# Optimization experiments

Hardware: AMD Instinct MI355X
Metric: run time of the kernel (lower is better)

## Reference

```python
import jax, jax.numpy as jnp
import numpy as np

S = 8192      # total patch tokens
NSEG = 8      # number of images/segments (equal length)
D = 1280      # embed dim
H = 16        # heads
HD = 80       # head dim
MLP = 3456    # swiglu hidden


def setup_inputs() -> dict:
    key = jax.random.key(0)
    ks = jax.random.split(key, 8)
    def w(k, shape):
        return jax.random.normal(k, shape, jnp.float32) * 0.02
    return {
        "x": jax.random.normal(ks[0], (S, 1, D), jnp.float32),
        "rotary_pos_emb": jax.random.uniform(ks[1], (S, HD // 2), jnp.float32) * 6.2831853,
        "cu_seqlens": jnp.arange(NSEG + 1, dtype=jnp.int32) * (S // NSEG),
        "norm1_w": jnp.ones((D,), jnp.float32), "norm1_b": jnp.zeros((D,), jnp.float32),
        "norm2_w": jnp.ones((D,), jnp.float32), "norm2_b": jnp.zeros((D,), jnp.float32),
        "w_qkv": w(ks[2], (3 * D, D)), "b_qkv": jnp.zeros((3 * D,), jnp.float32),
        "w_proj": w(ks[3], (D, D)), "b_proj": jnp.zeros((D,), jnp.float32),
        "w_gate": w(ks[4], (MLP, D)), "b_gate": jnp.zeros((MLP,), jnp.float32),
        "w_up": w(ks[5], (MLP, D)), "b_up": jnp.zeros((MLP,), jnp.float32),
        "w_down": w(ks[6], (D, MLP)), "b_down": jnp.zeros((D,), jnp.float32),
    }


def _ln(x, w, b, eps=1e-6):
    m = x.mean(-1, keepdims=True)
    v = ((x - m) ** 2).mean(-1, keepdims=True)
    return (x - m) * jax.lax.rsqrt(v + eps) * w + b


def _rope(x, cos, sin):
    # x: [B, S, H, HD]; cos/sin: [S, HD/2]; non-interleaved (chunk-halves) rotation
    c = jnp.concatenate([cos, cos], -1)[None, :, None, :]
    s = jnp.concatenate([sin, sin], -1)[None, :, None, :]
    x1, x2 = jnp.split(x, 2, -1)
    return x * c + jnp.concatenate([-x2, x1], -1) * s


def _forward(cu, x, freqs, norm1_w, norm1_b, norm2_w, norm2_b,
             w_qkv, b_qkv, w_proj, b_proj,
             w_gate, b_gate, w_up, b_up, w_down, b_down):
    S_, B, D_ = x.shape  # B == 1
    L = int(cu[1] - cu[0])          # equal-length segments
    nseg = len(cu) - 1
    h = _ln(x, norm1_w, norm1_b)
    qkv = h @ w_qkv.T + b_qkv                                   # [S, B, 3D]
    q, k, v = jnp.split(qkv, 3, -1)
    q, k, v = (t.reshape(S_, B, H, HD).transpose(1, 0, 2, 3) for t in (q, k, v))  # [B,S,H,d]
    cos, sin = jnp.cos(freqs), jnp.sin(freqs)
    q = _rope(q, cos, sin)
    k = _rope(k, cos, sin)
    # block-diagonal attention over cu_seqlens: fold segments into batch
    qs, ks_, vs = (t.reshape(B * nseg, L, H, HD) for t in (q, k, v))
    scale = 1.0 / np.float32(np.sqrt(HD))
    scores = jnp.einsum('blhd,bmhd->bhlm', qs, ks_) * scale     # [nseg,H,L,L]
    attn = jax.nn.softmax(scores, axis=-1)
    ctx = jnp.einsum('bhlm,bmhd->blhd', attn, vs)               # [nseg,L,H,d]
    ctx = ctx.reshape(B, S_, H * HD).transpose(1, 0, 2)         # [S,B,D]
    x = x + ctx @ w_proj.T + b_proj
    h2 = _ln(x, norm2_w, norm2_b)
    gate = jax.nn.silu(h2 @ w_gate.T + b_gate)
    up = h2 @ w_up.T + b_up
    return x + (gate * up) @ w_down.T + b_down


def reference(x, rotary_pos_emb, cu_seqlens, norm1_w, norm1_b, norm2_w, norm2_b,
              w_qkv, b_qkv, w_proj, b_proj, w_gate, b_gate, w_up, b_up,
              w_down, b_down):
    cu = np.asarray(cu_seqlens)
    return _forward(cu, x, rotary_pos_emb, norm1_w, norm1_b, norm2_w, norm2_b,
                    w_qkv, b_qkv, w_proj, b_proj,
                    w_gate, b_gate, w_up, b_up, w_down, b_down)
```

## Files before the change

kernel.cpp:

```cpp
#include <hip/hip_runtime.h>


#define S_TOK 8192
#define DIM   1280
#define NHEAD 16
#define HDIM  80
#define SEGLEN 1024
#define MLPD  3456

typedef __attribute__((ext_vector_type(8))) short bf16x8;
typedef __attribute__((ext_vector_type(8))) unsigned short u16x8;
typedef __attribute__((ext_vector_type(4))) float f32x4;

__device__ __forceinline__ float bf2f(unsigned short u) {
    unsigned int x = ((unsigned int)u) << 16;
    return __builtin_bit_cast(float, x);
}
__device__ __forceinline__ unsigned short f2bf(float f) {
    unsigned int x = __builtin_bit_cast(unsigned int, f);
    unsigned int r = x + 0x7fffu + ((x >> 16) & 1u);
    return (unsigned short)(r >> 16);
}

__device__ __forceinline__ void gload_lds16(const void* g, void* l) {
    __builtin_amdgcn_global_load_lds(
        (const __attribute__((address_space(1))) void*)g,
        (__attribute__((address_space(3))) void*)l, 16, 0, 0);
}

__device__ __forceinline__ int xcd_swz(int bid, int nwg) {
    const int q = nwg >> 3, r = nwg & 7;
    const int x = bid & 7, j = bid >> 3;
    return (x < r ? x * (q + 1) : r * (q + 1) + (x - r) * q) + j;
}

__global__ __launch_bounds__(256)
void f2b_kernel(const float* __restrict__ in, unsigned short* __restrict__ out, int n4)
{
    const int i = blockIdx.x * 256 + threadIdx.x;
    if (i >= n4) return;
    const float4 v = ((const float4*)in)[i];
    ushort4 o;
    o.x = f2bf(v.x); o.y = f2bf(v.y); o.z = f2bf(v.z); o.w = f2bf(v.w);
    ((ushort4*)out)[i] = o;
}

__global__ __launch_bounds__(256)
void ln_kernel(const float* __restrict__ xin,
               const float* __restrict__ w,
               const float* __restrict__ b,
               unsigned short* __restrict__ out)
{
    const int row = blockIdx.x;
    const int t = threadIdx.x;
    const size_t base = (size_t)row * DIM;
    float v[5];
#pragma unroll
    for (int i = 0; i < 5; ++i) v[i] = xin[base + t + i * 256];
    float s = 0.f, s2 = 0.f;
#pragma unroll
    for (int i = 0; i < 5; ++i) { s += v[i]; s2 += v[i] * v[i]; }
#pragma unroll
    for (int off = 32; off > 0; off >>= 1) {
        s  += __shfl_down(s, off);
        s2 += __shfl_down(s2, off);
    }
    __shared__ float rs[8];
    const int wave = t >> 6, lane = t & 63;
    if (lane == 0) { rs[wave] = s; rs[wave + 4] = s2; }
    __syncthreads();
    s  = rs[0] + rs[1] + rs[2] + rs[3];
    s2 = rs[4] + rs[5] + rs[6] + rs[7];
    const float mean = s * (1.f / DIM);
    const float var  = s2 * (1.f / DIM) - mean * mean;
    const float rstd = rsqrtf(var + 1e-6f);
#pragma unroll
    for (int i = 0; i < 5; ++i) {
        const int c = t + i * 256;
        out[base + c] = f2bf((v[i] - mean) * rstd * w[c] + b[c]);
    }
}

__global__ __launch_bounds__(256)
void rope_kernel(const unsigned short* __restrict__ qkv,
                 const float* __restrict__ rot,
                 unsigned short* __restrict__ qr,
                 unsigned short* __restrict__ kr)
{
    const int idx = blockIdx.x * 256 + threadIdx.x;
    const int s = idx / DIM, rem = idx % DIM;
    const int h = rem / HDIM, d = rem % HDIM;
    const int dd = (d < 40) ? d : d - 40;
    const float th = rot[s * 40 + dd];
    const float c = __cosf(th), sn = __sinf(th);
    const size_t base = (size_t)s * (3 * DIM) + h * HDIM;
    const int partner = (d < 40) ? d + 40 : d - 40;
    const float sgn = (d < 40) ? -1.f : 1.f;
    const float q  = bf2f(qkv[base + d]);
    const float k  = bf2f(qkv[DIM + base + d]);
    const float qp = bf2f(qkv[base + partner]);
    const float kp = bf2f(qkv[DIM + base + partner]);
    const float qo = q * c + sgn * qp * sn;
    const float ko = k * c + sgn * kp * sn;
    qr[idx] = f2bf(qo * 0.11180339887498949f);
    kr[idx] = f2bf(ko);
}

enum { EPI_BF16 = 0, EPI_PROJ = 1, EPI_DOWN = 3 };

template<int EPI>
__global__ __launch_bounds__(512)
void gemm2p(const unsigned short* __restrict__ A,
            const unsigned short* __restrict__ B,
            const float* __restrict__ bias,
            void* __restrict__ C,
            const void* __restrict__ aux,
            int M, int N, int K, int ntn)
{
    __shared__ __align__(16) unsigned short As[2][256 * 32];
    __shared__ __align__(16) unsigned short Bs[2][128 * 32];
    const int t = threadIdx.x;
    const int wave = t >> 6, lane = t & 63;
    const int m = lane & 15, g = lane >> 4;
    const int wr = wave >> 1, wc = wave & 1;
    const int wg = xcd_swz(blockIdx.x, gridDim.x);
    const int n0 = (wg % ntn) * 128;
    const int m0 = (wg / ntn) * 256;

    f32x4 acc[4][4] = {};
    const int nk = K >> 5;

    auto STAGE = [&](int b, int kt) {
        const int k0 = kt << 5;
#pragma unroll
        for (int i = 0; i < 2; ++i) {
            const int ch = i * 512 + t;
            const int row = ch >> 2, cc = ch & 3;
            gload_lds16(A + (size_t)(m0 + row) * K + k0 + cc * 8, &As[b][ch * 8]);
        }
        {
            const int row = t >> 2, cc = t & 3;
            gload_lds16(B + (size_t)(n0 + row) * K + k0 + cc * 8, &Bs[b][t * 8]);
        }
    };

    STAGE(0, 0);
    __syncthreads();
    int cur = 0;
    for (int kt = 0; kt < nk; ++kt) {
        if (kt + 1 < nk) STAGE(cur ^ 1, kt + 1);
        bf16x8 af[4], bfv[4];
#pragma unroll
        for (int mm = 0; mm < 4; ++mm)
            af[mm] = *(const bf16x8*)&As[cur][(wr * 64 + mm * 16 + m) * 32 + g * 8];
#pragma unroll
        for (int nn = 0; nn < 4; ++nn)
            bfv[nn] = *(const bf16x8*)&Bs[cur][(wc * 64 + nn * 16 + m) * 32 + g * 8];
#pragma unroll
        for (int mm = 0; mm < 4; ++mm)
#pragma unroll
            for (int nn = 0; nn < 4; ++nn)
                acc[mm][nn] = __builtin_amdgcn_mfma_f32_16x16x32_bf16(
                    af[mm], bfv[nn], acc[mm][nn], 0, 0, 0);
        __syncthreads();
        cur ^= 1;
    }

#pragma unroll
    for (int mm = 0; mm < 4; ++mm) {
        const int row = m0 + wr * 64 + mm * 16 + g * 4;
#pragma unroll
        for (int nn = 0; nn < 4; ++nn) {
            const int col = n0 + wc * 64 + nn * 16 + m;
            const float bv = bias[col];
#pragma unroll
            for (int i = 0; i < 4; ++i) {
                const int r = row + i;
                const float v = acc[mm][nn][i] + bv;
                const size_t idx = (size_t)r * N + col;
                if (EPI == EPI_BF16) {
                    ((unsigned short*)C)[idx] = f2bf(v);
                } else if (EPI == EPI_PROJ) {
                    const float xr = ((const float*)aux)[idx];
                    ((float*)C)[idx] = v + xr;
                } else {
                    const float xr = ((const float*)aux)[idx];
                    ((float*)C)[idx] = v + xr;
                }
            }
        }
    }
}

__global__ __launch_bounds__(512)
void gemm2p_gu(const unsigned short* __restrict__ A,
               const unsigned short* __restrict__ Bg,
               const unsigned short* __restrict__ Bu,
               const float* __restrict__ bg,
               const float* __restrict__ bu,
               unsigned short* __restrict__ C,
               int M, int N, int K, int ntn)
{
    __shared__ __align__(16) unsigned short As[2][256 * 32];
    __shared__ __align__(16) unsigned short Gs[2][128 * 32];
    __shared__ __align__(16) unsigned short Us[2][128 * 32];
    const int t = threadIdx.x;
    const int wave = t >> 6, lane = t & 63;
    const int m = lane & 15, g = lane >> 4;
    const int wr = wave >> 1, wc = wave & 1;
    const int wg = xcd_swz(blockIdx.x, gridDim.x);
    const int n0 = (wg % ntn) * 128;
    const int m0 = (wg / ntn) * 256;

    f32x4 accg[4][4] = {}, accu[4][4] = {};
    const int nk = K >> 5;

    auto STAGE = [&](int b, int kt) {
        const int k0 = kt << 5;
#pragma unroll
        for (int i = 0; i < 2; ++i) {
            const int ch = i * 512 + t;
            const int row = ch >> 2, cc = ch & 3;
            gload_lds16(A + (size_t)(m0 + row) * K + k0 + cc * 8, &As[b][ch * 8]);
        }
        {
            const int row = t >> 2, cc = t & 3;
            gload_lds16(Bg + (size_t)(n0 + row) * K + k0 + cc * 8, &Gs[b][t * 8]);
            gload_lds16(Bu + (size_t)(n0 + row) * K + k0 + cc * 8, &Us[b][t * 8]);
        }
    };

    STAGE(0, 0);
    __syncthreads();
    int cur = 0;
    for (int kt = 0; kt < nk; ++kt) {
        if (kt + 1 < nk) STAGE(cur ^ 1, kt + 1);
        bf16x8 af[4], gf[4], uf[4];
#pragma unroll
        for (int mm = 0; mm < 4; ++mm)
            af[mm] = *(const bf16x8*)&As[cur][(wr * 64 + mm * 16 + m) * 32 + g * 8];
#pragma unroll
        for (int nn = 0; nn < 4; ++nn) {
            gf[nn] = *(const bf16x8*)&Gs[cur][(wc * 64 + nn * 16 + m) * 32 + g * 8];
            uf[nn] = *(const bf16x8*)&Us[cur][(wc * 64 + nn * 16 + m) * 32 + g * 8];
        }
#pragma unroll
        for (int mm = 0; mm < 4; ++mm)
#pragma unroll
            for (int nn = 0; nn < 4; ++nn) {
                accg[mm][nn] = __builtin_amdgcn_mfma_f32_16x16x32_bf16(
                    af[mm], gf[nn], accg[mm][nn], 0, 0, 0);
                accu[mm][nn] = __builtin_amdgcn_mfma_f32_16x16x32_bf16(
                    af[mm], uf[nn], accu[mm][nn], 0, 0, 0);
            }
        __syncthreads();
        cur ^= 1;
    }

#pragma unroll
    for (int mm = 0; mm < 4; ++mm) {
        const int row = m0 + wr * 64 + mm * 16 + g * 4;
#pragma unroll
        for (int nn = 0; nn < 4; ++nn) {
            const int col = n0 + wc * 64 + nn * 16 + m;
            const float bgv = bg[col], buv = bu[col];
#pragma unroll
            for (int i = 0; i < 4; ++i) {
                const float gv = accg[mm][nn][i] + bgv;
                const float uv = accu[mm][nn][i] + buv;
                const float sg = gv / (1.f + __expf(-gv));
                C[(size_t)(row + i) * N + col] = f2bf(sg * uv);
            }
        }
    }
}

__global__ __launch_bounds__(256)
void attn_mfma_kernel(const unsigned short* __restrict__ qr,
                      const unsigned short* __restrict__ kr,
                      const unsigned short* __restrict__ qkv,
                      unsigned short* __restrict__ ctx)
{
    const int qt = blockIdx.x, hh = blockIdx.y, seg = blockIdx.z;
    const int t = threadIdx.x;
    const int w = t >> 6, lane = t & 63;
    const int m = lane & 15, g = lane >> 4;

    __shared__ __align__(16) unsigned short Ks[64 * 80];
    __shared__ __align__(16) unsigned short Vt[80 * 72];
    __shared__ __align__(16) unsigned short Ps[4][16 * 72];

    const int q0 = seg * SEGLEN + qt * 64 + w * 16;

    bf16x8 qa0, qa1, qa2 = {};
    {
        const unsigned short* qrow = qr + (size_t)(q0 + m) * DIM + hh * HDIM;
        qa0 = *(const bf16x8*)(qrow + 8 * g);
        qa1 = *(const bf16x8*)(qrow + 32 + 8 * g);
        if (g < 2) qa2 = *(const bf16x8*)(qrow + 64 + 8 * g);
    }

    f32x4 o[5] = {};
    float mrow[4], lrow[4];
#pragma unroll
    for (int i = 0; i < 4; ++i) { mrow[i] = -1e30f; lrow[i] = 0.f; }

    for (int kt = 0; kt < SEGLEN / 64; ++kt) {
        const int kbase = seg * SEGLEN + kt * 64;
#pragma unroll
        for (int i = 0; i < 2; ++i) {
            const int ch = t + 256 * i;
            const int row = ch / 10, c = ch % 10;
            gload_lds16(kr + (size_t)(kbase + row) * DIM + hh * HDIM + c * 8,
                        &Ks[ch * 8]);
        }
        if (t < 128) {
            const int ch = 512 + t;
            const int row = ch / 10, c = ch % 10;
            gload_lds16(kr + (size_t)(kbase + row) * DIM + hh * HDIM + c * 8,
                        &Ks[ch * 8]);
        }
#pragma unroll
        for (int i = 0; i < 3; ++i) {
            const int ch = t + 256 * i;
            if (ch < 640) {
                const int k = ch & 63, dc = ch >> 6;
                const u16x8 v = *(const u16x8*)(qkv +
                    (size_t)(kbase + k) * (3 * DIM) + 2 * DIM + hh * HDIM + dc * 8);
#pragma unroll
                for (int e = 0; e < 8; ++e)
                    Vt[(dc * 8 + e) * 72 + k] = v[e];
            }
        }
        __syncthreads();

        f32x4 s[4] = {};
#pragma unroll
        for (int nn = 0; nn < 4; ++nn) {
            const unsigned short* kb = &Ks[(16 * nn + m) * 80];
            const bf16x8 b0 = *(const bf16x8*)(kb + 8 * g);
            const bf16x8 b1 = *(const bf16x8*)(kb + 32 + 8 * g);
            bf16x8 b2 = {};
            if (g < 2) b2 = *(const bf16x8*)(kb + 64 + 8 * g);
            s[nn] = __builtin_amdgcn_mfma_f32_16x16x32_bf16(qa0, b0, s[nn], 0, 0, 0);
            s[nn] = __builtin_amdgcn_mfma_f32_16x16x32_bf16(qa1, b1, s[nn], 0, 0, 0);
            s[nn] = __builtin_amdgcn_mfma_f32_16x16x32_bf16(qa2, b2, s[nn], 0, 0, 0);
        }

#pragma unroll
        for (int i = 0; i < 4; ++i) {
            float mx = fmaxf(fmaxf(s[0][i], s[1][i]), fmaxf(s[2][i], s[3][i]));
            mx = fmaxf(mx, __shfl_xor(mx, 1));
            mx = fmaxf(mx, __shfl_xor(mx, 2));
            mx = fmaxf(mx, __shfl_xor(mx, 4));
            mx = fmaxf(mx, __shfl_xor(mx, 8));
            const float mn = fmaxf(mrow[i], mx);
            const float fs = __expf(mrow[i] - mn);
            float rs = 0.f;
#pragma unroll
            for (int nn = 0; nn < 4; ++nn) {
                const float p = __expf(s[nn][i] - mn);
                s[nn][i] = p;
                rs += p;
            }
            rs += __shfl_xor(rs, 1);
            rs += __shfl_xor(rs, 2);
            rs += __shfl_xor(rs, 4);
            rs += __shfl_xor(rs, 8);
            lrow[i] = lrow[i] * fs + rs;
            mrow[i] = mn;
#pragma unroll
            for (int df = 0; df < 5; ++df) o[df][i] *= fs;
        }

#pragma unroll
        for (int nn = 0; nn < 4; ++nn)
#pragma unroll
            for (int i = 0; i < 4; ++i)
                Ps[w][(4 * g + i) * 72 + 16 * nn + m] = f2bf(s[nn][i]);

        const bf16x8 pa0 = *(const bf16x8*)&Ps[w][m * 72 + 8 * g];
        const bf16x8 pa1 = *(const bf16x8*)&Ps[w][m * 72 + 32 + 8 * g];
#pragma unroll
        for (int df = 0; df < 5; ++df) {
            const unsigned short* vb = &Vt[(16 * df + m) * 72];
            const bf16x8 vb0 = *(const bf16x8*)(vb + 8 * g);
            const bf16x8 vb1 = *(const bf16x8*)(vb + 32 + 8 * g);
            o[df] = __builtin_amdgcn_mfma_f32_16x16x32_bf16(pa0, vb0, o[df], 0, 0, 0);
            o[df] = __builtin_amdgcn_mfma_f32_16x16x32_bf16(pa1, vb1, o[df], 0, 0, 0);
        }
        __syncthreads();
    }

#pragma unroll
    for (int i = 0; i < 4; ++i) {
        const float inv = 1.f / lrow[i];
        unsigned short* crow = ctx + (size_t)(q0 + 4 * g + i) * DIM + hh * HDIM;
#pragma unroll
        for (int df = 0; df < 5; ++df)
            crow[16 * df + m] = f2bf(o[df][i] * inv);
    }
}

extern "C" void kernel_launch(void* const* d_in, const int* in_sizes, int n_in,
                              void* d_out, int out_size, void* d_ws, size_t ws_size,
                              hipStream_t stream)
{
    const float* x      = (const float*)d_in[0];
    const float* rot    = (const float*)d_in[1];
    const float* n1w    = (const float*)d_in[3];
    const float* n1b    = (const float*)d_in[4];
    const float* n2w    = (const float*)d_in[5];
    const float* n2b    = (const float*)d_in[6];
    const float* w_qkv  = (const float*)d_in[7];
    const float* b_qkv  = (const float*)d_in[8];
    const float* w_proj = (const float*)d_in[9];
    const float* b_proj = (const float*)d_in[10];
    const float* w_gate = (const float*)d_in[11];
    const float* b_gate = (const float*)d_in[12];
    const float* w_up   = (const float*)d_in[13];
    const float* b_up   = (const float*)d_in[14];
    const float* w_down = (const float*)d_in[15];
    const float* b_down = (const float*)d_in[16];

    char* ws = (char*)d_ws;
    unsigned short* qkv  = (unsigned short*)(ws + 0);
    unsigned short* h    = (unsigned short*)(ws + 62914560ull);
    unsigned short* qr   = (unsigned short*)(ws + 83886080ull);
    unsigned short* kr   = (unsigned short*)(ws + 104857600ull);
    unsigned short* ctx  = (unsigned short*)(ws + 125829120ull);
    float*          x2   = (float*)(ws + 146800640ull);
    unsigned short* wqb  = (unsigned short*)(ws + 188743680ull);
    unsigned short* wpb  = (unsigned short*)(ws + 198574080ull);
    unsigned short* wgb  = (unsigned short*)(ws + 201850880ull);
    unsigned short* wub  = (unsigned short*)(ws + 210698240ull);
    unsigned short* wdb  = (unsigned short*)(ws + 219545600ull);
    unsigned short* gbuf = qkv;

    {
        const int nq = 3 * DIM * DIM / 4, np = DIM * DIM / 4, nm = MLPD * DIM / 4;
        f2b_kernel<<<(nq + 255) / 256, 256, 0, stream>>>(w_qkv,  wqb, nq);
        f2b_kernel<<<(np + 255) / 256, 256, 0, stream>>>(w_proj, wpb, np);
        f2b_kernel<<<(nm + 255) / 256, 256, 0, stream>>>(w_gate, wgb, nm);
        f2b_kernel<<<(nm + 255) / 256, 256, 0, stream>>>(w_up,   wub, nm);
        f2b_kernel<<<(nm + 255) / 256, 256, 0, stream>>>(w_down, wdb, nm);
    }

    ln_kernel<<<S_TOK, 256, 0, stream>>>(x, n1w, n1b, h);
    gemm2p<EPI_BF16><<<(3 * DIM / 128) * (S_TOK / 256), 512, 0, stream>>>(
        h, wqb, b_qkv, qkv, nullptr, S_TOK, 3 * DIM, DIM, 3 * DIM / 128);
    rope_kernel<<<(S_TOK * DIM) / 256, 256, 0, stream>>>(qkv, rot, qr, kr);
    attn_mfma_kernel<<<dim3(SEGLEN / 64, NHEAD, S_TOK / SEGLEN), 256, 0, stream>>>(
        qr, kr, qkv, ctx);
    gemm2p<EPI_PROJ><<<(DIM / 128) * (S_TOK / 256), 512, 0, stream>>>(
        ctx, wpb, b_proj, x2, x, S_TOK, DIM, DIM, DIM / 128);
    ln_kernel<<<S_TOK, 256, 0, stream>>>(x2, n2w, n2b, h);
    gemm2p_gu<<<(MLPD / 128) * (S_TOK / 256), 512, 0, stream>>>(
        h, wgb, wub, b_gate, b_up, gbuf, S_TOK, MLPD, DIM, MLPD / 128);
    gemm2p<EPI_DOWN><<<(DIM / 128) * (S_TOK / 256), 512, 0, stream>>>(
        gbuf, wdb, b_down, (float*)d_out, x2, S_TOK, DIM, MLPD, DIM / 128);
}
```

Baseline: 682.0 us.

## Rework GEMMs with 4-stage LDS pipeline, XOR swizzle, and larger per-wave tiles

Replaces the double-buffered GEMM kernels with a four-slot ring in dynamic shared memory, keeping three k-tiles of global-to-LDS loads in flight through explicit vmcnt waits. It also XOR-swizzles the LDS layout to cut bank conflicts, regroups the eight waves as 2x4 so each wave computes 128 rows with more MFMAs per fragment load, widens the QKV tile to 256 columns, and raises wave priority around the MFMA block. The larger LDS footprint (up to 128KB) and accumulator count may lower occupancy and raise register pressure.

Measured after the change: 677.6 us. Within noise of the previous version (-0.7%).

```diff
diff --git a/kernel.cpp b/kernel.cpp
--- a/kernel.cpp
+++ b/kernel.cpp
@@ -108,75 +108,98 @@
 
 enum { EPI_BF16 = 0, EPI_PROJ = 1, EPI_DOWN = 3 };
 
-template<int EPI>
+template<int EPI, int BN>
 __global__ __launch_bounds__(512)
-void gemm2p(const unsigned short* __restrict__ A,
+void gemm8p(const unsigned short* __restrict__ A,
             const unsigned short* __restrict__ B,
             const float* __restrict__ bias,
             void* __restrict__ C,
             const void* __restrict__ aux,
             int M, int N, int K, int ntn)
 {
-    __shared__ __align__(16) unsigned short As[2][256 * 32];
-    __shared__ __align__(16) unsigned short Bs[2][128 * 32];
+    constexpr int NF = BN / 64;
+    constexpr int BL = BN / 128;
+    extern __shared__ __align__(16) unsigned short lds[];
+    unsigned short* Ar = lds;
+    unsigned short* Br = lds + 4 * 8192;
+
     const int t = threadIdx.x;
-    const int wave = t >> 6, lane = t & 63;
+    const int w = t >> 6, lane = t & 63;
     const int m = lane & 15, g = lane >> 4;
-    const int wr = wave >> 1, wc = wave & 1;
+    const int gs = g ^ ((m >> 1) & 3);
+    const int wm = w >> 2, wn = w & 3;
     const int wg = xcd_swz(blockIdx.x, gridDim.x);
-    const int n0 = (wg % ntn) * 128;
+    const int n0 = (wg % ntn) * BN;
     const int m0 = (wg / ntn) * 256;
-
-    f32x4 acc[4][4] = {};
-    const int nk = K >> 5;
-
-    auto STAGE = [&](int b, int kt) {
-        const int k0 = kt << 5;
+    const int NP = K >> 5;
+
+    f32x4 acc[8][NF] = {};
+
+    auto STAGE = [&](int u) {
+        const int k0 = u << 5, us = u & 3;
 #pragma unroll
         for (int i = 0; i < 2; ++i) {
-            const int ch = i * 512 + t;
-            const int row = ch >> 2, cc = ch & 3;
-            gload_lds16(A + (size_t)(m0 + row) * K + k0 + cc * 8, &As[b][ch * 8]);
-        }
-        {
-            const int row = t >> 2, cc = t & 3;
-            gload_lds16(B + (size_t)(n0 + row) * K + k0 + cc * 8, &Bs[b][t * 8]);
+            const int c = i * 512 + t;
+            const int row = c >> 2, cc = (c & 3) ^ ((c >> 3) & 3);
+            gload_lds16(A + (size_t)(m0 + row) * K + k0 + cc * 8,
+                        &Ar[us * 8192 + c * 8]);
+        }
+#pragma unroll
+        for (int i = 0; i < BL; ++i) {
+            const int c = i * 512 + t;
+            const int row = c >> 2, cc = (c & 3) ^ ((c >> 3) & 3);
+            gload_lds16(B + (size_t)(n0 + row) * K + k0 + cc * 8,
+                        &Br[us * (BN * 32) + c * 8]);
         }
     };
 
-    STAGE(0, 0);
-    __syncthreads();
-    int cur = 0;
-    for (int kt = 0; kt < nk; ++kt) {
-        if (kt + 1 < nk) STAGE(cur ^ 1, kt + 1);
-        bf16x8 af[4], bfv[4];
-#pragma unroll
-        for (int mm = 0; mm < 4; ++mm)
-            af[mm] = *(const bf16x8*)&As[cur][(wr * 64 + mm * 16 + m) * 32 + g * 8];
-#pragma unroll
-        for (int nn = 0; nn < 4; ++nn)
-            bfv[nn] = *(const bf16x8*)&Bs[cur][(wc * 64 + nn * 16 + m) * 32 + g * 8];
-#pragma unroll
-        for (int mm = 0; mm < 4; ++mm)
-#pragma unroll
-            for (int nn = 0; nn < 4; ++nn)
-                acc[mm][nn] = __builtin_amdgcn_mfma_f32_16x16x32_bf16(
-                    af[mm], bfv[nn], acc[mm][nn], 0, 0, 0);
-        __syncthreads();
-        cur ^= 1;
-    }
-
-#pragma unroll
-    for (int mm = 0; mm < 4; ++mm) {
-        const int row = m0 + wr * 64 + mm * 16 + g * 4;
-#pragma unroll
-        for (int nn = 0; nn < 4; ++nn) {
-            const int col = n0 + wc * 64 + nn * 16 + m;
+    STAGE(0); STAGE(1); STAGE(2);
+    if constexpr (BL == 2) asm volatile("s_waitcnt vmcnt(8)" ::: "memory");
+    else                   asm volatile("s_waitcnt vmcnt(6)" ::: "memory");
+    __builtin_amdgcn_s_barrier();
+
+    for (int P = 0; P < NP; ++P) {
+        const int us = P & 3;
+        bf16x8 a[8], b[NF];
+#pragma unroll
+        for (int mf = 0; mf < 8; ++mf)
+            a[mf] = *(const bf16x8*)&Ar[us * 8192 + (wm * 128 + mf * 16 + m) * 32 + gs * 8];
+#pragma unroll
+        for (int nf = 0; nf < NF; ++nf)
+            b[nf] = *(const bf16x8*)&Br[us * (BN * 32) + (wn * (BN / 4) + nf * 16 + m) * 32 + gs * 8];
+        if (P + 3 < NP) {
+            STAGE(P + 3);
+            if constexpr (BL == 2) asm volatile("s_waitcnt vmcnt(8)" ::: "memory");
+            else                   asm volatile("s_waitcnt vmcnt(6)" ::: "memory");
+        } else if (P + 2 < NP) {
+            if constexpr (BL == 2) asm volatile("s_waitcnt vmcnt(4)" ::: "memory");
+            else                   asm volatile("s_waitcnt vmcnt(3)" ::: "memory");
+        } else if (P + 1 < NP) {
+            asm volatile("s_waitcnt vmcnt(0)" ::: "memory");
+        }
+        __builtin_amdgcn_s_barrier();
+        __builtin_amdgcn_s_setprio(1);
+#pragma unroll
+        for (int mf = 0; mf < 8; ++mf)
+#pragma unroll
+            for (int nf = 0; nf < NF; ++nf)
+                acc[mf][nf] = __builtin_amdgcn_mfma_f32_16x16x32_bf16(
+                    a[mf], b[nf], acc[mf][nf], 0, 0, 0);
+        __builtin_amdgcn_s_setprio(0);
+        __builtin_amdgcn_s_barrier();
+    }
+
+#pragma unroll
+    for (int mf = 0; mf < 8; ++mf) {
+        const int row = m0 + wm * 128 + mf * 16 + g * 4;
+#pragma unroll
+        for (int nf = 0; nf < NF; ++nf) {
+            const int col = n0 + wn * (BN / 4) + nf * 16 + m;
             const float bv = bias[col];
 #pragma unroll
             for (int i = 0; i < 4; ++i) {
                 const int r = row + i;
-                const float v = acc[mm][nn][i] + bv;
+                const float v = acc[mf][nf][i] + bv;
                 const size_t idx = (size_t)r * N + col;
                 if (EPI == EPI_BF16) {
                     ((unsigned short*)C)[idx] = f2bf(v);
@@ -193,7 +216,7 @@
 }
 
 __global__ __launch_bounds__(512)
-void gemm2p_gu(const unsigned short* __restrict__ A,
+void gemm8p_gu(const unsigned short* __restrict__ A,
                const unsigned short* __restrict__ Bg,
                const unsigned short* __restrict__ Bu,
                const float* __restrict__ bg,
@@ -201,73 +224,91 @@
                unsigned short* __restrict__ C,
                int M, int N, int K, int ntn)
 {
-    __shared__ __align__(16) unsigned short As[2][256 * 32];
-    __shared__ __align__(16) unsigned short Gs[2][128 * 32];
-    __shared__ __align__(16) unsigned short Us[2][128 * 32];
+    extern __shared__ __align__(16) unsigned short lds[];
+    unsigned short* Ar = lds;
+    unsigned short* Gr = lds + 4 * 8192;
+    unsigned short* Ur = Gr + 4 * 4096;
+
     const int t = threadIdx.x;
-    const int wave = t >> 6, lane = t & 63;
+    const int w = t >> 6, lane = t & 63;
     const int m = lane & 15, g = lane >> 4;
-    const int wr = wave >> 1, wc = wave & 1;
+    const int gs = g ^ ((m >> 1) & 3);
+    const int wm = w >> 2, wn = w & 3;
     const int wg = xcd_swz(blockIdx.x, gridDim.x);
     const int n0 = (wg % ntn) * 128;
     const int m0 = (wg / ntn) * 256;
-
-    f32x4 accg[4][4] = {}, accu[4][4] = {};
-    const int nk = K >> 5;
-
-    auto STAGE = [&](int b, int kt) {
-        const int k0 = kt << 5;
+    const int NP = K >> 5;
+
+    f32x4 accg[8][2] = {}, accu[8][2] = {};
+
+    auto STAGE = [&](int u) {
+        const int k0 = u << 5, us = u & 3;
 #pragma unroll
         for (int i = 0; i < 2; ++i) {
-            const int ch = i * 512 + t;
-            const int row = ch >> 2, cc = ch & 3;
-            gload_lds16(A + (size_t)(m0 + row) * K + k0 + cc * 8, &As[b][ch * 8]);
+            const int c = i * 512 + t;
+            const int row = c >> 2, cc = (c & 3) ^ ((c >> 3) & 3);
+            gload_lds16(A + (size_t)(m0 + row) * K + k0 + cc * 8,
+                        &Ar[us * 8192 + c * 8]);
         }
         {
-            const int row = t >> 2, cc = t & 3;
-            gload_lds16(Bg + (size_t)(n0 + row) * K + k0 + cc * 8, &Gs[b][t * 8]);
-            gload_lds16(Bu + (size_t)(n0 + row) * K + k0 + cc * 8, &Us[b][t * 8]);
+            const int c = t;
+            const int row = c >> 2, cc = (c & 3) ^ ((c >> 3) & 3);
+            gload_lds16(Bg + (size_t)(n0 + row) * K + k0 + cc * 8,
+                        &Gr[us * 4096 + c * 8]);
+            gload_lds16(Bu + (size_t)(n0 + row) * K + k0 + cc * 8,
+                        &Ur[us * 4096 + c * 8]);
         }
     };
 
-    STAGE(0, 0);
-    __syncthreads();
-    int cur = 0;
-    for (int kt = 0; kt < nk; ++kt) {
-        if (kt + 1 < nk) STAGE(cur ^ 1, kt + 1);
-        bf16x8 af[4], gf[4], uf[4];
-#pragma unroll
-        for (int mm = 0; mm < 4; ++mm)
-            af[mm] = *(const bf16x8*)&As[cur][(wr * 64 + mm * 16 + m) * 32 + g * 8];
-#pragma unroll
-        for (int nn = 0; nn < 4; ++nn) {
-            gf[nn] = *(const bf16x8*)&Gs[cur][(wc * 64 + nn * 16 + m) * 32 + g * 8];
-            uf[nn] = *(const bf16x8*)&Us[cur][(wc * 64 + nn * 16 + m) * 32 + g * 8];
-        }
-#pragma unroll
-        for (int mm = 0; mm < 4; ++mm)
-#pragma unroll
-            for (int nn = 0; nn < 4; ++nn) {
-                accg[mm][nn] = __builtin_amdgcn_mfma_f32_16x16x32_bf16(
-                    af[mm], gf[nn], accg[mm][nn], 0, 0, 0);
-                accu[mm][nn] = __builtin_amdgcn_mfma_f32_16x16x32_bf16(
-                    af[mm], uf[nn], accu[mm][nn], 0, 0, 0);
+    STAGE(0); STAGE(1); STAGE(2);
+    asm volatile("s_waitcnt vmcnt(8)" ::: "memory");
+    __builtin_amdgcn_s_barrier();
+
+    for (int P = 0; P < NP; ++P) {
+        const int us = P & 3;
+        bf16x8 a[8], bgf[2], buf[2];
+#pragma unroll
+        for (int mf = 0; mf < 8; ++mf)
+            a[mf] = *(const bf16x8*)&Ar[us * 8192 + (wm * 128 + mf * 16 + m) * 32 + gs * 8];
+#pragma unroll
+        for (int nf = 0; nf < 2; ++nf) {
+            bgf[nf] = *(const bf16x8*)&Gr[us * 4096 + (wn * 32 + nf * 16 + m) * 32 + gs * 8];
+            buf[nf] = *(const bf16x8*)&Ur[us * 4096 + (wn * 32 + nf * 16 + m) * 32 + gs * 8];
+        }
+        if (P + 3 < NP) {
+            STAGE(P + 3);
+            asm volatile("s_waitcnt vmcnt(8)" ::: "memory");
+        } else if (P + 2 < NP) {
+            asm volatile("s_waitcnt vmcnt(4)" ::: "memory");
+        } else if (P + 1 < NP) {
+            asm volatile("s_waitcnt vmcnt(0)" ::: "memory");
+        }
+        __builtin_amdgcn_s_barrier();
+        __builtin_amdgcn_s_setprio(1);
+#pragma unroll
+        for (int mf = 0; mf < 8; ++mf)
+#pragma unroll
+            for (int nf = 0; nf < 2; ++nf) {
+                accg[mf][nf] = __builtin_amdgcn_mfma_f32_16x16x32_bf16(
+                    a[mf], bgf[nf], accg[mf][nf], 0, 0, 0);
+                accu[mf][nf] = __builtin_amdgcn_mfma_f32_16x16x32_bf16(
+                    a[mf], buf[nf], accu[mf][nf], 0, 0, 0);
             }
-        __syncthreads();
-        cur ^= 1;
-    }
-
-#pragma unroll
-    for (int mm = 0; mm < 4; ++mm) {
-        const int row = m0 + wr * 64 + mm * 16 + g * 4;
-#pragma unroll
-        for (int nn = 0; nn < 4; ++nn) {
-            const int col = n0 + wc * 64 + nn * 16 + m;
+        __builtin_amdgcn_s_setprio(0);
+        __builtin_amdgcn_s_barrier();
+    }
+
+#pragma unroll
+    for (int mf = 0; mf < 8; ++mf) {
+        const int row = m0 + wm * 128 + mf * 16 + g * 4;
+#pragma unroll
+        for (int nf = 0; nf < 2; ++nf) {
+            const int col = n0 + wn * 32 + nf * 16 + m;
             const float bgv = bg[col], buv = bu[col];
 #pragma unroll
             for (int i = 0; i < 4; ++i) {
-                const float gv = accg[mm][nn][i] + bgv;
-                const float uv = accu[mm][nn][i] + buv;
+                const float gv = accg[mf][nf][i] + bgv;
+                const float uv = accu[mf][nf][i] + buv;
                 const float sg = gv / (1.f + __expf(-gv));
                 C[(size_t)(row + i) * N + col] = f2bf(sg * uv);
             }
@@ -437,6 +478,15 @@
     unsigned short* wdb  = (unsigned short*)(ws + 219545600ull);
     unsigned short* gbuf = qkv;
 
+    hipFuncSetAttribute(reinterpret_cast<const void*>(gemm8p<EPI_BF16, 256>),
+                        hipFuncAttributeMaxDynamicSharedMemorySize, 131072);
+    hipFuncSetAttribute(reinterpret_cast<const void*>(gemm8p<EPI_PROJ, 128>),
+                        hipFuncAttributeMaxDynamicSharedMemorySize, 98304);
+    hipFuncSetAttribute(reinterpret_cast<const void*>(gemm8p<EPI_DOWN, 128>),
+                        hipFuncAttributeMaxDynamicSharedMemorySize, 98304);
+    hipFuncSetAttribute(reinterpret_cast<const void*>(gemm8p_gu),
+                        hipFuncAttributeMaxDynamicSharedMemorySize, 131072);
+
     {
         const int nq = 3 * DIM * DIM / 4, np = DIM * DIM / 4, nm = MLPD * DIM / 4;
         f2b_kernel<<<(nq + 255) / 256, 256, 0, stream>>>(w_qkv,  wqb, nq);
@@ -447,16 +497,16 @@
     }
 
     ln_kernel<<<S_TOK, 256, 0, stream>>>(x, n1w, n1b, h);
-    gemm2p<EPI_BF16><<<(3 * DIM / 128) * (S_TOK / 256), 512, 0, stream>>>(
-        h, wqb, b_qkv, qkv, nullptr, S_TOK, 3 * DIM, DIM, 3 * DIM / 128);
+    gemm8p<EPI_BF16, 256><<<(3 * DIM / 256) * (S_TOK / 256), 512, 131072, stream>>>(
+        h, wqb, b_qkv, qkv, nullptr, S_TOK, 3 * DIM, DIM, 3 * DIM / 256);
     rope_kernel<<<(S_TOK * DIM) / 256, 256, 0, stream>>>(qkv, rot, qr, kr);
     attn_mfma_kernel<<<dim3(SEGLEN / 64, NHEAD, S_TOK / SEGLEN), 256, 0, stream>>>(
         qr, kr, qkv, ctx);
-    gemm2p<EPI_PROJ><<<(DIM / 128) * (S_TOK / 256), 512, 0, stream>>>(
+    gemm8p<EPI_PROJ, 128><<<(DIM / 128) * (S_TOK / 256), 512, 98304, stream>>>(
         ctx, wpb, b_proj, x2, x, S_TOK, DIM, DIM, DIM / 128);
     ln_kernel<<<S_TOK, 256, 0, stream>>>(x2, n2w, n2b, h);
-    gemm2p_gu<<<(MLPD / 128) * (S_TOK / 256), 512, 0, stream>>>(
+    gemm8p_gu<<<(MLPD / 128) * (S_TOK / 256), 512, 131072, stream>>>(
         h, wgb, wub, b_gate, b_up, gbuf, S_TOK, MLPD, DIM, MLPD / 128);
-    gemm2p<EPI_DOWN><<<(DIM / 128) * (S_TOK / 256), 512, 0, stream>>>(
+    gemm8p<EPI_DOWN, 128><<<(DIM / 128) * (S_TOK / 256), 512, 98304, stream>>>(
         gbuf, wdb, b_down, (float*)d_out, x2, S_TOK, DIM, MLPD, DIM / 128);
 }
```
